# Kernel tuning notes

Hardware: AMD Instinct MI355X
Metric: run time of the kernel (lower is better)

Reference implementation:

```python
import jax, jax.numpy as jnp
import numpy as np

N_NODES = 50000
N_EDGES = 600000
FEAT = 128
N_LAYERS = 4


def setup_inputs() -> dict:
    key = jax.random.key(0)
    ks = jax.random.split(key, 7)
    feats = jax.random.normal(ks[0], (N_NODES, FEAT), dtype=jnp.float32)
    src = jax.random.randint(ks[1], (N_EDGES,), 0, N_NODES)
    dst = jax.random.randint(ks[2], (N_EDGES,), 0, N_NODES)
    s = 1.0 / np.sqrt(FEAT)  # torch Linear default init range
    theta_w = jax.random.uniform(ks[3], (N_LAYERS, FEAT, FEAT), jnp.float32, -s, s)
    theta_b = jax.random.uniform(ks[4], (N_LAYERS, FEAT), jnp.float32, -s, s)
    phi_w = jax.random.uniform(ks[5], (N_LAYERS, FEAT, FEAT), jnp.float32, -s, s)
    phi_b = jax.random.uniform(ks[6], (N_LAYERS, FEAT), jnp.float32, -s, s)
    return {"feats": feats, "src": src, "dst": dst,
            "theta_w": theta_w, "theta_b": theta_b,
            "phi_w": phi_w, "phi_b": phi_b}


def _edgeconv(x, src, dst, tw, tb, pw, pb):
    # EdgeConv (Wang et al. 2018): out_i = max_{(j->i) in E} theta(x_j - x_i) + phi(x_i)
    phi = x @ pw.T + pb                       # [N, F] node-level linear (avoid per-edge recompute)
    diff = x[src] - x[dst]                    # [E, F] gather
    msg = diff @ tw.T + tb + phi[dst]         # [E, F]
    agg = jax.ops.segment_max(msg, dst, num_segments=x.shape[0])  # [N, F]
    # nodes with no incoming edges get -inf from segment_max; zero them (DGL convention)
    return jnp.where(jnp.isneginf(agg), jnp.zeros_like(agg), agg)


def reference(feats, src, dst, theta_w, theta_b, phi_w, phi_b):
    x = feats
    for l in range(N_LAYERS):
        x = _edgeconv(x, src, dst, theta_w[l], theta_b[l], phi_w[l], phi_b[l])
        x = jax.nn.relu(x)
    return x
```

## Files before the change

kernel.cpp:

```cpp
#include <hip/hip_runtime.h>

#define FEAT 128
#define SLABS 4

typedef __attribute__((ext_vector_type(8))) _Float16 f16x8;
typedef __attribute__((ext_vector_type(2))) _Float16 f16x2;
typedef __attribute__((ext_vector_type(4))) float f32x4;

static __device__ __forceinline__ int wave_incl_scan(int v, int lane) {
#pragma unroll
    for (int off = 1; off < 64; off <<= 1) {
        int u = __shfl_up(v, off, 64);
        if (lane >= off) v += u;
    }
    return v;
}


__global__ void prep_kernel(const int* __restrict__ src, const int* __restrict__ dst,
                            int* __restrict__ deg4, int* __restrict__ erank,
                            int E, int slab_size,
                            const float* __restrict__ tw, const float* __restrict__ pw,
                            const float* __restrict__ tb, const float* __restrict__ pb,
                            _Float16* __restrict__ wt, _Float16* __restrict__ wp,
                            float* __restrict__ bsum, int wn, int nbias,
                            const float* __restrict__ x, _Float16* __restrict__ x16, int xn4,
                            int hb, int wb) {
    int bid = blockIdx.x;
    if (bid < hb) {
        int e = bid * 256 + threadIdx.x;
        if (e < E) {
            int sl = src[e] / slab_size;
            erank[e] = atomicAdd(&deg4[dst[e] * SLABS + sl], 1);
        }
    } else if (bid < hb + wb) {
        int i = (bid - hb) * 256 + threadIdx.x;
        if (i < wn) { wt[i] = (_Float16)tw[i]; wp[i] = (_Float16)pw[i]; }
        if (i < nbias) bsum[i] = tb[i] + pb[i];
    } else {
        int i = (bid - hb - wb) * 256 + threadIdx.x;
        if (i < xn4) {
            float4 v = ((const float4*)x)[i];
            f16x2 a, b;
            a[0] = (_Float16)v.x; a[1] = (_Float16)v.y;
            b[0] = (_Float16)v.z; b[1] = (_Float16)v.w;
            ((f16x2*)x16)[i * 2] = a;
            ((f16x2*)x16)[i * 2 + 1] = b;
        }
    }
}


__global__ __launch_bounds__(1024) void scan1_kernel(const int* __restrict__ deg,
                                                     int* __restrict__ row_ptr,
                                                     int* __restrict__ bsum, int N4) {
    int i = blockIdx.x * 1024 + threadIdx.x;
    int lane = threadIdx.x & 63;
    int w = threadIdx.x >> 6;
    int v = (i < N4) ? deg[i] : 0;
    int inc = wave_incl_scan(v, lane);
    __shared__ int wsum[16];
    if (lane == 63) wsum[w] = inc;
    __syncthreads();
    if (w == 0) {
        int s = (lane < 16) ? wsum[lane] : 0;
        int si = wave_incl_scan(s, lane);
        if (lane < 16) wsum[lane] = si - s;
    }
    __syncthreads();
    int exc = inc - v + wsum[w];
    if (i < N4) row_ptr[i] = exc;
    if (threadIdx.x == 1023) bsum[blockIdx.x] = exc + v;
}

__global__ __launch_bounds__(1024) void scan2_kernel(const int* __restrict__ bsum,
                                                     int* __restrict__ boff,
                                                     int* __restrict__ row_ptr,
                                                     int nb, int N4, int E) {
    int tid = threadIdx.x;
    int lane = tid & 63;
    int w = tid >> 6;
    int v = (tid < nb) ? bsum[tid] : 0;
    int inc = wave_incl_scan(v, lane);
    __shared__ int wsum[16];
    if (lane == 63) wsum[w] = inc;
    __syncthreads();
    if (w == 0) {
        int s = (lane < 16) ? wsum[lane] : 0;
        int si = wave_incl_scan(s, lane);
        if (lane < 16) wsum[lane] = si - s;
    }
    __syncthreads();
    if (tid < nb) boff[tid] = inc - v + wsum[w];
    if (tid == 0) row_ptr[N4] = E;
}

__global__ void scan3_kernel(int* __restrict__ row_ptr, const int* __restrict__ boff, int N4) {
    int i = blockIdx.x * blockDim.x + threadIdx.x;
    if (i < N4) row_ptr[i] += boff[i >> 10];
}


static __device__ __forceinline__ void gemm_body(
        int bx, int nslab,
        const _Float16* __restrict__ x16,
        const _Float16* __restrict__ wt, const _Float16* __restrict__ wp,
        const float* __restrict__ bias,
        _Float16* __restrict__ t16, _Float16* __restrict__ q16, int M) {
    int lane = threadIdx.x & 63;
    int l16 = lane & 15;
    int quad = lane >> 4;
    int cn0 = (threadIdx.x >> 6) * 32;

    f16x8 bt[2][4], bp[2][4];
    float biasv[2];
#pragma unroll
    for (int ct = 0; ct < 2; ++ct) {
        int col = cn0 + ct * 16 + l16;
        biasv[ct] = bias[col];
#pragma unroll
        for (int kk = 0; kk < 4; ++kk) {
            int k = kk * 32 + quad * 8;
            bt[ct][kk] = *(const f16x8*)(wt + (size_t)col * FEAT + k);
            bp[ct][kk] = *(const f16x8*)(wp + (size_t)col * FEAT + k);
        }
    }

    int rbase0 = bx * (nslab * 16);
#pragma unroll 1
    for (int rs = 0; rs < nslab; ++rs) {
        int rbase = rbase0 + rs * 16;
        int row = rbase + l16;
        int rowc = (row < M) ? row : (M - 1);
        f16x8 a[4];
#pragma unroll
        for (int kk = 0; kk < 4; ++kk)
            a[kk] = *(const f16x8*)(x16 + (size_t)rowc * FEAT + kk * 32 + quad * 8);

        f32x4 accT[2] = {{0.f, 0.f, 0.f, 0.f}, {0.f, 0.f, 0.f, 0.f}};
        f32x4 accP[2] = {{0.f, 0.f, 0.f, 0.f}, {0.f, 0.f, 0.f, 0.f}};
#pragma unroll
        for (int kk = 0; kk < 4; ++kk) {
#pragma unroll
            for (int ct = 0; ct < 2; ++ct) {
                accT[ct] = __builtin_amdgcn_mfma_f32_16x16x32_f16(a[kk], bt[ct][kk], accT[ct], 0, 0, 0);
                accP[ct] = __builtin_amdgcn_mfma_f32_16x16x32_f16(a[kk], bp[ct][kk], accP[ct], 0, 0, 0);
            }
        }
#pragma unroll
        for (int ct = 0; ct < 2; ++ct) {
            int col = cn0 + ct * 16 + l16;
#pragma unroll
            for (int r = 0; r < 4; ++r) {
                int ro = rbase + quad * 4 + r;
                if (ro < M) {
                    t16[(size_t)ro * FEAT + col] = (_Float16)accT[ct][r];
                    q16[(size_t)ro * FEAT + col] =
                        (_Float16)(accP[ct][r] - accT[ct][r] + biasv[ct]);
                }
            }
        }
    }
}

__global__ __launch_bounds__(256) void mfma_gemm_kernel(
        const _Float16* __restrict__ x16,
        const _Float16* __restrict__ wt, const _Float16* __restrict__ wp,
        const float* __restrict__ bias,
        _Float16* __restrict__ t16, _Float16* __restrict__ q16, int M) {
    gemm_body(blockIdx.x, 4, x16, wt, wp, bias, t16, q16, M);
}

__global__ __launch_bounds__(256) void fused0_kernel(
        const _Float16* __restrict__ x16,
        const _Float16* __restrict__ wt, const _Float16* __restrict__ wp,
        const float* __restrict__ bias,
        _Float16* __restrict__ t16, _Float16* __restrict__ q16, int M, int gb,
        const int* __restrict__ src, const int* __restrict__ dst,
        const int* __restrict__ row_ptr4, const int* __restrict__ erank,
        int* __restrict__ esrc, int E, int slab_size) {
    if ((int)blockIdx.x < gb) {
        gemm_body(blockIdx.x, 8, x16, wt, wp, bias, t16, q16, M);
    } else {
        int e = (blockIdx.x - gb) * 256 + threadIdx.x;
        if (e < E) {
            int s = src[e];
            int key = dst[e] * SLABS + s / slab_size;
            esrc[row_ptr4[key] + erank[e]] = s;
        }
    }
}


static __device__ __forceinline__ f16x8 vmax8(f16x8 a, f16x8 b) {
#pragma unroll
    for (int i = 0; i < 8; ++i) a[i] = (a[i] > b[i]) ? a[i] : b[i];
    return a;
}

static __device__ __forceinline__ f16x8 shfl_xor8(f16x8 v, int m) {
    union { f16x8 h; int i[4]; } u, r;
    u.h = v;
#pragma unroll
    for (int d = 0; d < 4; ++d) r.i[d] = __shfl_xor(u.i[d], m, 64);
    return r.h;
}

__global__ __launch_bounds__(256) void agg_kernel(
        const _Float16* __restrict__ t16, const _Float16* __restrict__ q16,
        const int* __restrict__ row_ptr4, const int* __restrict__ esrc,
        float* __restrict__ outf, _Float16* __restrict__ ox, int N) {
    int wv = threadIdx.x >> 6;
    int lane = threadIdx.x & 63;
    int node = blockIdx.x * 4 + wv;
    if (node >= N) return;

    int g = lane >> 4;
    int c = lane & 15;

    int beg = row_ptr4[node * SLABS];
    int end = row_ptr4[node * SLABS + SLABS];
    int cnt = end - beg;

    f16x2 qv = *(const f16x2*)(q16 + (size_t)node * FEAT + c * 8 + g * 2);

    const _Float16 NEGINF = (_Float16)(-65504.0f);
    f16x8 m0, m1;
#pragma unroll
    for (int i = 0; i < 8; ++i) { m0[i] = NEGINF; m1[i] = NEGINF; }

    for (int cb = 0; cb < cnt; cb += 64) {
        int lim = cnt - cb; if (lim > 64) lim = 64;
        int a = beg + cb + (lane < lim ? lane : 0);
        int myidx = esrc[a];
        for (int base = 0; base < lim; base += 8) {
            int e0 = base + g;     if (e0 >= lim) e0 = 0;
            int e1 = base + 4 + g; if (e1 >= lim) e1 = 0;
            int i0 = __shfl(myidx, e0, 64);
            int i1 = __shfl(myidx, e1, 64);
            f16x8 v0 = *(const f16x8*)(t16 + (size_t)i0 * FEAT + c * 8);
            f16x8 v1 = *(const f16x8*)(t16 + (size_t)i1 * FEAT + c * 8);
            m0 = vmax8(m0, v0);
            m1 = vmax8(m1, v1);
        }
    }

    f16x8 mm = vmax8(m0, m1);
    mm = vmax8(mm, shfl_xor8(mm, 16));
    mm = vmax8(mm, shfl_xor8(mm, 32));

    union { f16x8 h; int i[4]; } um; um.h = mm;
    int w01 = (g & 1) ? um.i[1] : um.i[0];
    int w23 = (g & 1) ? um.i[3] : um.i[2];
    int w = (g & 2) ? w23 : w01;
    union { int i; f16x2 h; } uw; uw.i = w;

    float o0 = fmaxf((float)uw.h[0] + (float)qv[0], 0.f);
    float o1 = fmaxf((float)uw.h[1] + (float)qv[1], 0.f);

    if (outf) {
        float2 ov = make_float2(o0, o1);
        *(float2*)(outf + (size_t)node * FEAT + c * 8 + g * 2) = ov;
    }
    if (ox) {
        f16x2 oh; oh[0] = (_Float16)o0; oh[1] = (_Float16)o1;
        *(f16x2*)(ox + (size_t)node * FEAT + c * 8 + g * 2) = oh;
    }
}


extern "C" void kernel_launch(void* const* d_in, const int* in_sizes, int n_in,
                              void* d_out, int out_size, void* d_ws, size_t ws_size,
                              hipStream_t stream) {
    const float* feats   = (const float*)d_in[0];
    const int*   src     = (const int*)d_in[1];
    const int*   dst     = (const int*)d_in[2];
    const float* theta_w = (const float*)d_in[3];
    const float* theta_b = (const float*)d_in[4];
    const float* phi_w   = (const float*)d_in[5];
    const float* phi_b   = (const float*)d_in[6];

    const int N = in_sizes[0] / FEAT;
    const int E = in_sizes[1];
    const int L = in_sizes[3] / (FEAT * FEAT);
    const int N4 = N * SLABS;
    const int slab_size = (N + SLABS - 1) / SLABS;

    char* ws = (char*)d_ws;
    size_t off = 0;
    auto alloc = [&](size_t bytes) -> void* {
        void* ptr = ws + off;
        off = (off + bytes + 255) & ~(size_t)255;
        return ptr;
    };
    _Float16* t16 = (_Float16*)alloc((size_t)N * FEAT * 2);
    _Float16* q16 = (_Float16*)alloc((size_t)N * FEAT * 2);
    _Float16* x16 = (_Float16*)alloc((size_t)N * FEAT * 2);
    _Float16* wt16 = (_Float16*)alloc((size_t)L * FEAT * FEAT * 2);
    _Float16* wp16 = (_Float16*)alloc((size_t)L * FEAT * FEAT * 2);
    float* bsum_b = (float*)alloc((size_t)L * FEAT * sizeof(float));
    int* deg4     = (int*)alloc((size_t)N4 * sizeof(int));
    int* row_ptr4 = (int*)alloc((size_t)(N4 + 1) * sizeof(int));
    int* erank    = (int*)alloc((size_t)E * sizeof(int));
    int* esrc     = (int*)alloc((size_t)E * sizeof(int));
    int* bsum     = (int*)alloc(2048 * sizeof(int));
    int* boff     = (int*)alloc(2048 * sizeof(int));
    (void)ws_size;

    hipMemsetAsync(deg4, 0, (size_t)N4 * sizeof(int), stream);

    int eb = (E + 255) / 256;
    int wn = L * FEAT * FEAT;
    int wb = (wn + 255) / 256;
    int xn4 = N * FEAT / 4;
    int xb = (xn4 + 255) / 256;
    prep_kernel<<<eb + wb + xb, 256, 0, stream>>>(
        src, dst, deg4, erank, E, slab_size,
        theta_w, phi_w, theta_b, phi_b, wt16, wp16, bsum_b, wn, L * FEAT,
        feats, x16, xn4, eb, wb);

    int nb = (N4 + 1023) >> 10;
    scan1_kernel<<<nb, 1024, 0, stream>>>(deg4, row_ptr4, bsum, N4);
    scan2_kernel<<<1, 1024, 0, stream>>>(bsum, boff, row_ptr4, nb, N4, E);
    scan3_kernel<<<(N4 + 255) / 256, 256, 0, stream>>>(row_ptr4, boff, N4);

    int gb = (N + 127) / 128;
    int gb2 = (N + 63) / 64;
    int ab = (N + 3) / 4;
    for (int l = 0; l < L; ++l) {
        if (l == 0) {
            fused0_kernel<<<gb + eb, 256, 0, stream>>>(
                x16, wt16, wp16, bsum_b, t16, q16, N, gb,
                src, dst, row_ptr4, erank, esrc, E, slab_size);
        } else {
            mfma_gemm_kernel<<<gb2, 256, 0, stream>>>(
                x16,
                wt16 + (size_t)l * FEAT * FEAT,
                wp16 + (size_t)l * FEAT * FEAT,
                bsum_b + (size_t)l * FEAT,
                t16, q16, N);
        }

        bool last = (l == L - 1);
        agg_kernel<<<ab, 256, 0, stream>>>(
            t16, q16, row_ptr4, esrc,
            last ? (float*)d_out : nullptr,
            last ? nullptr : x16,
            N);
    }
}
```

Before: 317.1 us.

## Fuse aggregation with next-layer GEMM and fold scan offsets into readers

Each middle layer's max-aggregation now writes its 16-node tile into LDS and immediately runs the next layer's MFMA projection, using ping-pong t/q buffers. This avoids the global x16 write and read and the separate GEMM launch. The third scan pass is removed by adding block offsets at every row_ptr read. The trade-off is that weights are reloaded per small block and each wave aggregates four nodes serially, which may reduce latency hiding in the gather.

```diff
diff --git a/kernel.cpp b/kernel.cpp
--- a/kernel.cpp
+++ b/kernel.cpp
@@ -91,13 +91,9 @@
         if (lane < 16) wsum[lane] = si - s;
     }
     __syncthreads();
-    if (tid < nb) boff[tid] = inc - v + wsum[w];
-    if (tid == 0) row_ptr[N4] = E;
-}
-
-__global__ void scan3_kernel(int* __restrict__ row_ptr, const int* __restrict__ boff, int N4) {
-    int i = blockIdx.x * blockDim.x + threadIdx.x;
-    if (i < N4) row_ptr[i] += boff[i >> 10];
+    int b = inc - v + wsum[w];
+    if (tid <= nb) boff[tid] = b;
+    if (tid == (N4 >> 10)) row_ptr[N4] = E - b;
 }
 
 
@@ -163,21 +159,14 @@
     }
 }
 
-__global__ __launch_bounds__(256) void mfma_gemm_kernel(
-        const _Float16* __restrict__ x16,
-        const _Float16* __restrict__ wt, const _Float16* __restrict__ wp,
-        const float* __restrict__ bias,
-        _Float16* __restrict__ t16, _Float16* __restrict__ q16, int M) {
-    gemm_body(blockIdx.x, 4, x16, wt, wp, bias, t16, q16, M);
-}
-
 __global__ __launch_bounds__(256) void fused0_kernel(
         const _Float16* __restrict__ x16,
         const _Float16* __restrict__ wt, const _Float16* __restrict__ wp,
         const float* __restrict__ bias,
         _Float16* __restrict__ t16, _Float16* __restrict__ q16, int M, int gb,
         const int* __restrict__ src, const int* __restrict__ dst,
-        const int* __restrict__ row_ptr4, const int* __restrict__ erank,
+        const int* __restrict__ row_ptr4, const int* __restrict__ boff,
+        const int* __restrict__ erank,
         int* __restrict__ esrc, int E, int slab_size) {
     if ((int)blockIdx.x < gb) {
         gemm_body(blockIdx.x, 8, x16, wt, wp, bias, t16, q16, M);
@@ -186,7 +175,7 @@
         if (e < E) {
             int s = src[e];
             int key = dst[e] * SLABS + s / slab_size;
-            esrc[row_ptr4[key] + erank[e]] = s;
+            esrc[row_ptr4[key] + boff[key >> 10] + erank[e]] = s;
         }
     }
 }
@@ -206,24 +195,9 @@
     return r.h;
 }
 
-__global__ __launch_bounds__(256) void agg_kernel(
-        const _Float16* __restrict__ t16, const _Float16* __restrict__ q16,
-        const int* __restrict__ row_ptr4, const int* __restrict__ esrc,
-        float* __restrict__ outf, _Float16* __restrict__ ox, int N) {
-    int wv = threadIdx.x >> 6;
-    int lane = threadIdx.x & 63;
-    int node = blockIdx.x * 4 + wv;
-    if (node >= N) return;
-
-    int g = lane >> 4;
-    int c = lane & 15;
-
-    int beg = row_ptr4[node * SLABS];
-    int end = row_ptr4[node * SLABS + SLABS];
-    int cnt = end - beg;
-
-    f16x2 qv = *(const f16x2*)(q16 + (size_t)node * FEAT + c * 8 + g * 2);
-
+static __device__ __forceinline__ f16x8 gather_max(
+        const _Float16* __restrict__ t16, const int* __restrict__ esrc,
+        int beg, int cnt, int lane, int g, int c) {
     const _Float16 NEGINF = (_Float16)(-65504.0f);
     f16x8 m0, m1;
 #pragma unroll
@@ -248,24 +222,118 @@
     f16x8 mm = vmax8(m0, m1);
     mm = vmax8(mm, shfl_xor8(mm, 16));
     mm = vmax8(mm, shfl_xor8(mm, 32));
-
+    return mm;
+}
+
+static __device__ __forceinline__ f16x2 slot_pair(f16x8 mm, int g) {
     union { f16x8 h; int i[4]; } um; um.h = mm;
     int w01 = (g & 1) ? um.i[1] : um.i[0];
     int w23 = (g & 1) ? um.i[3] : um.i[2];
     int w = (g & 2) ? w23 : w01;
     union { int i; f16x2 h; } uw; uw.i = w;
-
-    float o0 = fmaxf((float)uw.h[0] + (float)qv[0], 0.f);
-    float o1 = fmaxf((float)uw.h[1] + (float)qv[1], 0.f);
-
-    if (outf) {
-        float2 ov = make_float2(o0, o1);
-        *(float2*)(outf + (size_t)node * FEAT + c * 8 + g * 2) = ov;
-    }
-    if (ox) {
+    return uw.h;
+}
+
+
+__global__ __launch_bounds__(256) void fusedagg_kernel(
+        const _Float16* __restrict__ t16, const _Float16* __restrict__ q16,
+        const int* __restrict__ row_ptr4, const int* __restrict__ boff,
+        const int* __restrict__ esrc,
+        const _Float16* __restrict__ wt, const _Float16* __restrict__ wp,
+        const float* __restrict__ bias,
+        _Float16* __restrict__ tn, _Float16* __restrict__ qn, int N) {
+    __shared__ _Float16 xl[16 * FEAT];
+    int wv = threadIdx.x >> 6;
+    int lane = threadIdx.x & 63;
+    int g = lane >> 4;
+    int c = lane & 15;
+    int node0 = blockIdx.x * 16;
+
+#pragma unroll 1
+    for (int k = 0; k < 4; ++k) {
+        int nr = wv * 4 + k;
+        int node = node0 + nr;
+        float o0 = 0.f, o1 = 0.f;
+        if (node < N) {
+            int bi = node * SLABS;
+            int beg = row_ptr4[bi] + boff[bi >> 10];
+            int end = row_ptr4[bi + SLABS] + boff[(bi + SLABS) >> 10];
+            f16x2 qv = *(const f16x2*)(q16 + (size_t)node * FEAT + c * 8 + g * 2);
+            f16x8 mm = gather_max(t16, esrc, beg, end - beg, lane, g, c);
+            f16x2 mp = slot_pair(mm, g);
+            o0 = fmaxf((float)mp[0] + (float)qv[0], 0.f);
+            o1 = fmaxf((float)mp[1] + (float)qv[1], 0.f);
+        }
         f16x2 oh; oh[0] = (_Float16)o0; oh[1] = (_Float16)o1;
-        *(f16x2*)(ox + (size_t)node * FEAT + c * 8 + g * 2) = oh;
-    }
+        int byteoff = (nr * 256 + c * 16 + g * 4) ^ ((nr & 7) << 4);
+        *(f16x2*)((char*)xl + byteoff) = oh;
+    }
+    __syncthreads();
+
+    int l16 = lane & 15;
+    int quad = lane >> 4;
+    int cn0 = wv * 32;
+    f16x8 a[4];
+#pragma unroll
+    for (int kk = 0; kk < 4; ++kk) {
+        int byteoff = (l16 * 256 + kk * 64 + quad * 16) ^ ((l16 & 7) << 4);
+        a[kk] = *(const f16x8*)((const char*)xl + byteoff);
+    }
+#pragma unroll 1
+    for (int ct = 0; ct < 2; ++ct) {
+        int col = cn0 + ct * 16 + l16;
+        float bv = bias[col];
+        f16x8 fb[4];
+#pragma unroll
+        for (int kk = 0; kk < 4; ++kk)
+            fb[kk] = *(const f16x8*)(wt + (size_t)col * FEAT + kk * 32 + quad * 8);
+        f32x4 accT = {0.f, 0.f, 0.f, 0.f};
+#pragma unroll
+        for (int kk = 0; kk < 4; ++kk)
+            accT = __builtin_amdgcn_mfma_f32_16x16x32_f16(a[kk], fb[kk], accT, 0, 0, 0);
+#pragma unroll
+        for (int kk = 0; kk < 4; ++kk)
+            fb[kk] = *(const f16x8*)(wp + (size_t)col * FEAT + kk * 32 + quad * 8);
+        f32x4 accP = {0.f, 0.f, 0.f, 0.f};
+#pragma unroll
+        for (int kk = 0; kk < 4; ++kk)
+            accP = __builtin_amdgcn_mfma_f32_16x16x32_f16(a[kk], fb[kk], accP, 0, 0, 0);
+#pragma unroll
+        for (int r = 0; r < 4; ++r) {
+            int ro = node0 + quad * 4 + r;
+            if (ro < N) {
+                tn[(size_t)ro * FEAT + col] = (_Float16)accT[r];
+                qn[(size_t)ro * FEAT + col] = (_Float16)(accP[r] - accT[r] + bv);
+            }
+        }
+    }
+}
+
+__global__ __launch_bounds__(256) void agg_kernel(
+        const _Float16* __restrict__ t16, const _Float16* __restrict__ q16,
+        const int* __restrict__ row_ptr4, const int* __restrict__ boff,
+        const int* __restrict__ esrc,
+        float* __restrict__ outf, int N) {
+    int wv = threadIdx.x >> 6;
+    int lane = threadIdx.x & 63;
+    int node = blockIdx.x * 4 + wv;
+    if (node >= N) return;
+
+    int g = lane >> 4;
+    int c = lane & 15;
+
+    int bi = node * SLABS;
+    int beg = row_ptr4[bi] + boff[bi >> 10];
+    int end = row_ptr4[bi + SLABS] + boff[(bi + SLABS) >> 10];
+
+    f16x2 qv = *(const f16x2*)(q16 + (size_t)node * FEAT + c * 8 + g * 2);
+    f16x8 mm = gather_max(t16, esrc, beg, end - beg, lane, g, c);
+    f16x2 mp = slot_pair(mm, g);
+
+    float o0 = fmaxf((float)mp[0] + (float)qv[0], 0.f);
+    float o1 = fmaxf((float)mp[1] + (float)qv[1], 0.f);
+    float2 ov = make_float2(o0, o1);
+    *(float2*)(outf + (size_t)node * FEAT + c * 8 + g * 2) = ov;
 }
 
 
@@ -293,8 +361,12 @@
         off = (off + bytes + 255) & ~(size_t)255;
         return ptr;
     };
-    _Float16* t16 = (_Float16*)alloc((size_t)N * FEAT * 2);
-    _Float16* q16 = (_Float16*)alloc((size_t)N * FEAT * 2);
+    _Float16* tbuf[2];
+    _Float16* qbuf[2];
+    tbuf[0] = (_Float16*)alloc((size_t)N * FEAT * 2);
+    tbuf[1] = (_Float16*)alloc((size_t)N * FEAT * 2);
+    qbuf[0] = (_Float16*)alloc((size_t)N * FEAT * 2);
+    qbuf[1] = (_Float16*)alloc((size_t)N * FEAT * 2);
     _Float16* x16 = (_Float16*)alloc((size_t)N * FEAT * 2);
     _Float16* wt16 = (_Float16*)alloc((size_t)L * FEAT * FEAT * 2);
     _Float16* wp16 = (_Float16*)alloc((size_t)L * FEAT * FEAT * 2);
@@ -322,30 +394,24 @@
     int nb = (N4 + 1023) >> 10;
     scan1_kernel<<<nb, 1024, 0, stream>>>(deg4, row_ptr4, bsum, N4);
     scan2_kernel<<<1, 1024, 0, stream>>>(bsum, boff, row_ptr4, nb, N4, E);
-    scan3_kernel<<<(N4 + 255) / 256, 256, 0, stream>>>(row_ptr4, boff, N4);
 
     int gb = (N + 127) / 128;
-    int gb2 = (N + 63) / 64;
+    fused0_kernel<<<gb + eb, 256, 0, stream>>>(
+        x16, wt16, wp16, bsum_b, tbuf[0], qbuf[0], N, gb,
+        src, dst, row_ptr4, boff, erank, esrc, E, slab_size);
+
+    int fb = (N + 15) / 16;
+    for (int l = 0; l + 1 < L; ++l) {
+        fusedagg_kernel<<<fb, 256, 0, stream>>>(
+            tbuf[l & 1], qbuf[l & 1], row_ptr4, boff, esrc,
+            wt16 + (size_t)(l + 1) * FEAT * FEAT,
+            wp16 + (size_t)(l + 1) * FEAT * FEAT,
+            bsum_b + (size_t)(l + 1) * FEAT,
+            tbuf[(l + 1) & 1], qbuf[(l + 1) & 1], N);
+    }
+
     int ab = (N + 3) / 4;
-    for (int l = 0; l < L; ++l) {
-        if (l == 0) {
-            fused0_kernel<<<gb + eb, 256, 0, stream>>>(
-                x16, wt16, wp16, bsum_b, t16, q16, N, gb,
-                src, dst, row_ptr4, erank, esrc, E, slab_size);
-        } else {
-            mfma_gemm_kernel<<<gb2, 256, 0, stream>>>(
-                x16,
-                wt16 + (size_t)l * FEAT * FEAT,
-                wp16 + (size_t)l * FEAT * FEAT,
-                bsum_b + (size_t)l * FEAT,
-                t16, q16, N);
-        }
-
-        bool last = (l == L - 1);
-        agg_kernel<<<ab, 256, 0, stream>>>(
-            t16, q16, row_ptr4, esrc,
-            last ? (float*)d_out : nullptr,
-            last ? nullptr : x16,
-            N);
-    }
-}
+    agg_kernel<<<ab, 256, 0, stream>>>(
+        tbuf[(L - 1) & 1], qbuf[(L - 1) & 1], row_ptr4, boff, esrc,
+        (float*)d_out, N);
+}
```

Result: faster. 310.8 us (-2.0%).
